# Kernel optimization log

Hardware: AMD Instinct MI355X
Metric: run time of the kernel (lower is better)

The kernel has to match this reference:

```python
import jax, jax.numpy as jnp
import numpy as np

B, C, F, T = 4, 64, 64, 128
IC = 32  # inter_channels = C // 2
EPS = 1e-5  # BatchNorm eps


def _conv1x1(x, w, b=None):
    # x: (B, Cin, H, W), w: (Cout, Cin)
    y = jnp.einsum('bchw,oc->bohw', x, w)
    if b is not None:
        y = y + b[None, :, None, None]
    return y


def _maxpool2(x):
    b, c, h, w = x.shape
    return x.reshape(b, c, h // 2, 2, w // 2, 2).max(axis=(3, 5))


def _pos_score(fsz, tsz, h2_w):
    # positional encoding is (fpos, tpos) in [0,1]; the 2->1 conv head makes the
    # pos_delta contribution separable: score(n,m) = s(n) - s(m)
    fpos = jnp.linspace(0.0, 1.0, fsz)
    tpos = jnp.linspace(0.0, 1.0, tsz)
    return (h2_w[0] * fpos[:, None] + h2_w[1] * tpos[None, :]).reshape(-1)


def setup_inputs() -> dict:
    key = jax.random.key(0)
    ks = jax.random.split(key, 16)
    s = 0.05
    inp = {
        'x': jax.random.normal(ks[0], (B, C, F, T), dtype=jnp.float32),
        'psi_w': jax.random.normal(ks[1], (IC, C)) * s,
        'psi_b': jax.random.normal(ks[2], (IC,)) * s,
        'theta_w': jax.random.normal(ks[3], (IC, C)) * s,
        'theta_b': jax.random.normal(ks[4], (IC,)) * s,
        'phi_w': jax.random.normal(ks[5], (IC, C)) * s,
        'phi_b': jax.random.normal(ks[6], (IC,)) * s,
        'h0_w': jax.random.normal(ks[7], (IC,)) * s,
        'h1_w': jax.random.normal(ks[8], (IC,)) * s,
        'h2_w': jax.random.normal(ks[9], (2,)) * s,
        'W_w': jax.random.normal(ks[10], (C, IC + 1)) * s,
        'W_b': jax.random.normal(ks[11], (C,)) * s,
        'bn_gamma': jax.random.normal(ks[12], (C,)) * s + 1.0,
        'bn_beta': jax.random.normal(ks[13], (C,)) * s,
        'bn_mean': jax.random.normal(ks[14], (C,)) * s,
        'bn_var': jax.random.uniform(ks[15], (C,), minval=0.5, maxval=1.5),
    }
    return inp


def reference(x, psi_w, psi_b, theta_w, theta_b, phi_w, phi_b,
              h0_w, h1_w, h2_w, W_w, W_b, bn_gamma, bn_beta, bn_mean, bn_var):
    Bs, Cs, Fs, Ts = x.shape
    N = Fs * Ts
    M = (Fs // 2) * (Ts // 2)

    psi_x = _maxpool2(_conv1x1(x, psi_w, psi_b))      # (B, IC, F/2, T/2)
    theta_x = _conv1x1(x, theta_w, theta_b)           # (B, IC, F, T)
    phi_x = _maxpool2(_conv1x1(x, phi_w, phi_b))      # (B, IC, F/2, T/2)

    # additive attention scores: relu(head0(theta) + head1(phi) + head2(pos_delta))
    t_score = jnp.einsum('bcft,c->bft', theta_x, h0_w).reshape(Bs, N)   # (B, N)
    p_score = jnp.einsum('bcft,c->bft', phi_x, h1_w).reshape(Bs, M)     # (B, M)
    a = _pos_score(Fs, Ts, h2_w)             # (N,) query pos contribution
    bpos = _pos_score(Fs // 2, Ts // 2, h2_w)  # (M,) key pos contribution
    f = jax.nn.relu((t_score + a[None, :])[:, :, None]
                    + (p_score - bpos[None, :])[:, None, :])  # (B, N, M)

    f_div = f / jnp.asarray(M, f.dtype)
    psi_flat = psi_x.reshape(Bs, IC, M)
    y = jnp.einsum('bnm,bcm->bcn', f_div, psi_flat).reshape(Bs, IC, Fs, Ts)

    # r_structure_type='zero' -> structure feature is zeros (1 extra channel)
    structure = jnp.zeros((Bs, 1, Fs, Ts), dtype=y.dtype)
    y = jnp.concatenate([y, structure], axis=1)       # (B, IC+1, F, T)

    wy = _conv1x1(y, W_w, W_b)                        # (B, C, F, T)
    inv = bn_gamma / jnp.sqrt(bn_var + EPS)
    wy = wy * inv[None, :, None, None] + (bn_beta - bn_mean * inv)[None, :, None, None]
    return wy + x
```

## Files before the change

### kernel.cpp

```cpp
#include <hip/hip_runtime.h>

#define B_ 4
#define C_ 64
#define F_ 64
#define T_ 128
#define IC_ 32
#define N_ 8192
#define M_ 2048

#define OFF_U      0
#define OFF_Z      32768
#define OFF_V      557056
#define OFF_VS     565248
#define OFF_Q01    573440
#define WS_FLOATS  1622528

__device__ __align__(16) float g_ws[WS_FLOATS];
__device__ int g_perm[B_ * M_];

__global__ __launch_bounds__(256) void k1(
    const float* __restrict__ x,
    const float* __restrict__ psi_w, const float* __restrict__ psi_b,
    const float* __restrict__ theta_w, const float* __restrict__ theta_b,
    const float* __restrict__ phi_w, const float* __restrict__ phi_b,
    const float* __restrict__ h0_w, const float* __restrict__ h1_w,
    const float* __restrict__ h2_w, const float* __restrict__ W_w)
{
    float* __restrict__ ws = g_ws;
    __shared__ __align__(16) float xs[4096];
    __shared__ __align__(16) float pw[2048];
    __shared__ __align__(16) float fw[2048];
    __shared__ __align__(16) float Wl[2048];
    __shared__ __align__(16) float pt[512];
    __shared__ float wt_l[64];

    const int tid = threadIdx.x;
    const int bid = blockIdx.x;
    const int b = bid >> 7;
    const int rem = bid & 127;
    const int fh = rem >> 2;
    const int q = rem & 3;
    const int c0 = q * 32;

    for (int idx = tid; idx < 1024; idx += 256) {
        const int c = idx >> 4, r2 = (idx >> 3) & 1, t4 = idx & 7;
        const float4 v = *(const float4*)&x[(((size_t)b * 64 + c) * 64 + (2 * fh + r2)) * 128 + c0 + 4 * t4];
        *(float4*)&xs[c * 64 + r2 * 32 + 4 * t4] = v;
    }
    for (int idx = tid; idx < 2048; idx += 256) {
        const int c4 = idx >> 7, o = (idx >> 2) & 31, j = idx & 3;
        pw[idx] = psi_w[o * 64 + 4 * c4 + j];
        fw[idx] = phi_w[o * 64 + 4 * c4 + j];
        const int c4w = idx >> 8, o64 = (idx >> 2) & 63, jw = idx & 3;
        Wl[idx] = W_w[o64 * 33 + 4 * c4w + jw];
    }
    if (tid < 64) {
        float acc = 0.f;
        for (int o2 = 0; o2 < 32; ++o2)
            acc += h0_w[o2] * theta_w[o2 * 64 + tid];
        wt_l[tid] = acc;
    }
    __syncthreads();

    const float h20 = h2_w[0], h21 = h2_w[1];

    {
        const int o = tid & 31, g = tid >> 5;
        const float pb = psi_b[o], fb = phi_b[o], h1 = h1_w[o];
        const float4* pw4 = (const float4*)pw;
        const float4* fw4 = (const float4*)fw;
        const float4* xs4 = (const float4*)xs;
        float sp[2][4] = {{0,0,0,0},{0,0,0,0}};
        float sf[2][4] = {{0,0,0,0},{0,0,0,0}};
        for (int c4 = 0; c4 < 16; ++c4) {
            const float4 pv = pw4[c4 * 32 + o];
            const float4 fv = fw4[c4 * 32 + o];
            const float* pvf = (const float*)&pv;
            const float* fvf = (const float*)&fv;
#pragma unroll
            for (int j = 0; j < 4; ++j) {
                const int c = 4 * c4 + j;
                const float4 r0 = xs4[c * 16 + g];
                const float4 r1 = xs4[c * 16 + 8 + g];
                const float wp = pvf[j], wf = fvf[j];
                sp[0][0] += wp * r0.x; sp[0][1] += wp * r0.y;
                sp[0][2] += wp * r1.x; sp[0][3] += wp * r1.y;
                sp[1][0] += wp * r0.z; sp[1][1] += wp * r0.w;
                sp[1][2] += wp * r1.z; sp[1][3] += wp * r1.w;
                sf[0][0] += wf * r0.x; sf[0][1] += wf * r0.y;
                sf[0][2] += wf * r1.x; sf[0][3] += wf * r1.y;
                sf[1][0] += wf * r0.z; sf[1][1] += wf * r0.w;
                sf[1][2] += wf * r1.z; sf[1][3] += wf * r1.w;
            }
        }
#pragma unroll
        for (int h = 0; h < 2; ++h) {
            const int hc = 2 * g + h;
            const float psiv = fmaxf(fmaxf(sp[h][0], sp[h][1]), fmaxf(sp[h][2], sp[h][3])) + pb;
            const float phiv = fmaxf(fmaxf(sf[h][0], sf[h][1]), fmaxf(sf[h][2], sf[h][3])) + fb;
            const int m = fh * 64 + q * 16 + hc;
            pt[hc * 32 + o] = psiv;
            float tv = h1 * phiv;
            for (int mask = 1; mask < 32; mask <<= 1)
                tv += __shfl_xor(tv, mask, 64);
            if (o == 0) {
                const float bpos = h20 * (fh * (1.0f / 31.0f))
                                 + h21 * ((q * 16 + hc) * (1.0f / 63.0f));
                ws[OFF_V + b * 2048 + m] = tv - bpos;
            }
        }
    }
    __syncthreads();

    {
        const int op = tid & 63, mseg = tid >> 6;
        const float4* Wl4 = (const float4*)Wl;
        const float4* pt4 = (const float4*)pt;
        float4 wreg[8];
#pragma unroll
        for (int c4 = 0; c4 < 8; ++c4)
            wreg[c4] = Wl4[c4 * 64 + op];
#pragma unroll
        for (int j = 0; j < 4; ++j) {
            const int ml = mseg * 4 + j;
            float acc = 0.f;
#pragma unroll
            for (int c4 = 0; c4 < 8; ++c4) {
                const float4 pv = pt4[ml * 8 + c4];
                acc += wreg[c4].x * pv.x + wreg[c4].y * pv.y
                     + wreg[c4].z * pv.z + wreg[c4].w * pv.w;
            }
            const int m = fh * 64 + q * 16 + ml;
            ws[OFF_Z + ((size_t)b * 2048 + m) * 64 + op] = acc;
        }
    }

    if (tid < 64) {
        const int r2 = tid >> 5, tl = tid & 31;
        float acc = 0.f;
        for (int c = 0; c < 64; ++c)
            acc += xs[c * 64 + r2 * 32 + tl] * wt_l[c];
        float tb_ = 0.f;
        for (int o2 = 0; o2 < 32; ++o2)
            tb_ += h0_w[o2] * theta_b[o2];
        const int f = 2 * fh + r2, tt = c0 + tl;
        const int n = f * 128 + tt;
        const float a = h20 * (f * (1.0f / 63.0f)) + h21 * (tt * (1.0f / 127.0f));
        ws[OFF_U + b * 8192 + n] = acc + tb_ + a;
    }
}

__global__ __launch_bounds__(256) void k2()
{
    float* __restrict__ ws = g_ws;
    __shared__ __align__(16) float vl[2048];
    __shared__ int part[256];
    const int tid = threadIdx.x;
    const int b = blockIdx.x >> 7, chunk = blockIdx.x & 127;
    const float* v = ws + OFF_V + b * 2048;
    for (int i = tid; i < 2048; i += 256) vl[i] = v[i];
    __syncthreads();

    const int ml = tid >> 4;
    const int jq = tid & 15;
    const int m = chunk * 16 + ml;
    const float vm = vl[m];
    int cnt = 0;
    const float4* v4 = (const float4*)vl;
#pragma unroll 4
    for (int i = 0; i < 32; ++i) {
        const int j4 = jq + 16 * i;
        const float4 vv = v4[j4];
        const int jb = j4 * 4;
        cnt += (vv.x > vm) || (vv.x == vm && (jb    ) < m);
        cnt += (vv.y > vm) || (vv.y == vm && (jb + 1) < m);
        cnt += (vv.z > vm) || (vv.z == vm && (jb + 2) < m);
        cnt += (vv.w > vm) || (vv.w == vm && (jb + 3) < m);
    }
    part[tid] = cnt;
    __syncthreads();
    if (tid < 16) {
        int r = 0;
#pragma unroll
        for (int j = 0; j < 16; ++j) r += part[tid * 16 + j];
        ws[OFF_VS + b * 2048 + r] = vl[chunk * 16 + tid];
        g_perm[b * 2048 + r] = chunk * 16 + tid;
    }
}

__global__ __launch_bounds__(512) void k3()
{
    float* __restrict__ ws = g_ws;
    __shared__ float wt0[8], wt1[8];
    const int tid = threadIdx.x;
    const int b = blockIdx.x >> 6, o = blockIdx.x & 63;

    const int* perm = g_perm + b * 2048;
    const float* vs = ws + OFF_VS + b * 2048;
    const float* zg = ws + OFF_Z + (size_t)b * 2048 * 64 + o;

    float zl[4], vlv[4];
    float s0 = 0.f, s1 = 0.f;
    const int base = tid * 4;
#pragma unroll
    for (int qq = 0; qq < 4; ++qq) {
        const int i = base + qq;
        const int mp = perm[i];
        const float z = zg[(size_t)mp * 64];
        const float vv = vs[i];
        zl[qq] = z; vlv[qq] = vv;
        s0 += z; s1 += vv * z;
    }

    float w0 = s0, w1 = s1;
    const int lane = tid & 63, wv = tid >> 6;
#pragma unroll
    for (int off = 1; off < 64; off <<= 1) {
        const float t0_ = __shfl_up(w0, off, 64);
        const float t1_ = __shfl_up(w1, off, 64);
        if (lane >= off) { w0 += t0_; w1 += t1_; }
    }
    if (lane == 63) { wt0[wv] = w0; wt1[wv] = w1; }
    __syncthreads();
    float base0 = 0.f, base1 = 0.f;
    for (int w = 0; w < wv; ++w) { base0 += wt0[w]; base1 += wt1[w]; }
    float r0 = w0 + base0 - s0, r1 = w1 + base1 - s1;

    float2* Q01 = (float2*)(ws + OFF_Q01) + (size_t)b * 2049 * 64;
#pragma unroll
    for (int qq = 0; qq < 4; ++qq) {
        r0 += zl[qq]; r1 += vlv[qq] * zl[qq];
        float2 p; p.x = r0; p.y = r1;
        Q01[(size_t)(base + qq + 1) * 64 + o] = p;
    }
    if (tid == 0) { float2 z2; z2.x = 0.f; z2.y = 0.f; Q01[o] = z2; }
}

__global__ __launch_bounds__(512) void k4(
    const float* __restrict__ x,
    const float* __restrict__ W_b,
    const float* __restrict__ bn_g, const float* __restrict__ bn_b,
    const float* __restrict__ bn_m, const float* __restrict__ bn_v,
    float* __restrict__ out)
{
    const float* __restrict__ ws = g_ws;
    __shared__ __align__(16) float vsl[2048];
    __shared__ float tileb[64 * 65];
    __shared__ int karr[64];
    __shared__ float uarr[64];

    const int tid = threadIdx.x;
    const int b = blockIdx.x >> 7, tile = blockIdx.x & 127;
    const int n0 = tile * 64;

    const float* vs = ws + OFF_VS + b * 2048;
    *(float4*)&vsl[tid * 4] = *(const float4*)&vs[tid * 4];
    __syncthreads();

    if (tid < 64) {
        const float u = ws[OFF_U + b * 8192 + n0 + tid];
        const float thr = -u;
        int lo = 0, hi = 2048;
        while (lo < hi) {
            const int mid = (lo + hi) >> 1;
            if (vsl[mid] > thr) lo = mid + 1; else hi = mid;
        }
        karr[tid] = lo;
        uarr[tid] = u;
    }
    __syncthreads();

    const int lane = tid & 63, w = tid >> 6;
    const float inv = bn_g[lane] * __frsqrt_rn(bn_v[lane] + 1e-5f);
    const float sft = W_b[lane] * inv + bn_b[lane] - bn_m[lane] * inv;
    const float2* Q01 = (const float2*)(ws + OFF_Q01) + (size_t)b * 2049 * 64;

    for (int nl = w; nl < 64; nl += 8) {
        const int k = karr[nl];
        const float u = uarr[nl];
        const float2 qv = Q01[(size_t)k * 64 + lane];
        const float raw = (u * qv.x + qv.y) * (1.0f / 2048.0f);
        tileb[lane * 65 + nl] = raw * inv + sft;
    }
    __syncthreads();

    for (int idx = tid; idx < 2048; idx += 512) {
        const int o = idx >> 5, j2 = idx & 31;
        const size_t gi = ((size_t)b * 64 + o) * 8192 + n0 + 2 * j2;
        const float2 xv = *(const float2*)&x[gi];
        float2 r;
        r.x = tileb[o * 65 + 2 * j2] + xv.x;
        r.y = tileb[o * 65 + 2 * j2 + 1] + xv.y;
        *(float2*)&out[gi] = r;
    }
}

extern "C" void kernel_launch(void* const* d_in, const int* in_sizes, int n_in,
                              void* d_out, int out_size, void* d_ws, size_t ws_size,
                              hipStream_t stream)
{
    (void)in_sizes; (void)n_in; (void)out_size; (void)d_ws; (void)ws_size;
    const float* x       = (const float*)d_in[0];
    const float* psi_w   = (const float*)d_in[1];
    const float* psi_b   = (const float*)d_in[2];
    const float* theta_w = (const float*)d_in[3];
    const float* theta_b = (const float*)d_in[4];
    const float* phi_w   = (const float*)d_in[5];
    const float* phi_b   = (const float*)d_in[6];
    const float* h0_w    = (const float*)d_in[7];
    const float* h1_w    = (const float*)d_in[8];
    const float* h2_w    = (const float*)d_in[9];
    const float* W_w     = (const float*)d_in[10];
    const float* W_b     = (const float*)d_in[11];
    const float* bn_g    = (const float*)d_in[12];
    const float* bn_b    = (const float*)d_in[13];
    const float* bn_m    = (const float*)d_in[14];
    const float* bn_v    = (const float*)d_in[15];
    float* out = (float*)d_out;

    k1<<<dim3(512), dim3(256), 0, stream>>>(x, psi_w, psi_b, theta_w, theta_b,
                                            phi_w, phi_b, h0_w, h1_w, h2_w, W_w);
    k2<<<dim3(512), dim3(256), 0, stream>>>();
    k3<<<dim3(256), dim3(512), 0, stream>>>();
    k4<<<dim3(512), dim3(512), 0, stream>>>(x, W_b, bn_g, bn_b, bn_m, bn_v, out);
}
```

Baseline: 120.2 us.

## Use bf16 MFMA for psi/phi and Z projections in k1 with swizzled LDS

Rewrites the first kernel to convert x and the weights to bf16 in swizzled shared memory and compute the psi/phi 1x1 convolutions and the W projection with 16x16x32 bf16 MFMA instructions instead of scalar FMA loops. Each block now covers 128 pixels, so the grid is halved. The Z workspace is transposed to channel-major so the gather in k3 reads contiguous rows per channel. This lowers arithmetic and LDS cost but brings bf16 rounding into the intermediate features, which can affect accuracy.

```diff
diff --git a/kernel.cpp b/kernel.cpp
--- a/kernel.cpp
+++ b/kernel.cpp
@@ -18,6 +18,23 @@
 __device__ __align__(16) float g_ws[WS_FLOATS];
 __device__ int g_perm[B_ * M_];
 
+typedef __attribute__((ext_vector_type(8))) short short8_t;
+typedef __attribute__((ext_vector_type(4))) float f32x4;
+
+__device__ __forceinline__ unsigned short f2bf(float f) {
+    unsigned b = __float_as_uint(f);
+    b += 0x7fffu + ((b >> 16) & 1u);
+    return (unsigned short)(b >> 16);
+}
+__device__ __forceinline__ float bf2f(unsigned short h) {
+    return __uint_as_float(((unsigned)h) << 16);
+}
+
+#define XSIDX(p, c)  ((((p) * 64) + (c)) ^ (((p) & 7) << 3))
+#define WAIDX(o, c)  ((((o) * 64) + (c)) ^ (((o) & 7) << 3))
+#define WZIDX(o, c)  ((((o) * 32) + (c)) ^ (((o) & 3) << 3))
+#define PSIDX(p, c)  ((((p) * 32) + (c)) ^ (((p) & 3) << 3))
+
 __global__ __launch_bounds__(256) void k1(
     const float* __restrict__ x,
     const float* __restrict__ psi_w, const float* __restrict__ psi_b,
@@ -27,126 +44,160 @@
     const float* __restrict__ h2_w, const float* __restrict__ W_w)
 {
     float* __restrict__ ws = g_ws;
-    __shared__ __align__(16) float xs[4096];
-    __shared__ __align__(16) float pw[2048];
-    __shared__ __align__(16) float fw[2048];
-    __shared__ __align__(16) float Wl[2048];
-    __shared__ __align__(16) float pt[512];
-    __shared__ float wt_l[64];
+    __shared__ __align__(16) unsigned short XS[128 * 64];
+    __shared__ __align__(16) unsigned short WA[64 * 64];
+    __shared__ __align__(16) unsigned short WZ[64 * 32];
+    __shared__ __align__(16) unsigned short PS[32 * 32];
+    __shared__ __align__(16) float pb[64];
+    __shared__ __align__(16) float h1l[32];
+    __shared__ __align__(16) float wtl[64];
+    __shared__ float vtmp[2][32];
 
     const int tid = threadIdx.x;
     const int bid = blockIdx.x;
-    const int b = bid >> 7;
-    const int rem = bid & 127;
-    const int fh = rem >> 2;
-    const int q = rem & 3;
-    const int c0 = q * 32;
-
-    for (int idx = tid; idx < 1024; idx += 256) {
-        const int c = idx >> 4, r2 = (idx >> 3) & 1, t4 = idx & 7;
-        const float4 v = *(const float4*)&x[(((size_t)b * 64 + c) * 64 + (2 * fh + r2)) * 128 + c0 + 4 * t4];
-        *(float4*)&xs[c * 64 + r2 * 32 + 4 * t4] = v;
-    }
-    for (int idx = tid; idx < 2048; idx += 256) {
-        const int c4 = idx >> 7, o = (idx >> 2) & 31, j = idx & 3;
-        pw[idx] = psi_w[o * 64 + 4 * c4 + j];
-        fw[idx] = phi_w[o * 64 + 4 * c4 + j];
-        const int c4w = idx >> 8, o64 = (idx >> 2) & 63, jw = idx & 3;
-        Wl[idx] = W_w[o64 * 33 + 4 * c4w + jw];
-    }
+    const int b = bid >> 6;
+    const int rem = bid & 63;
+    const int fh = rem >> 1;
+    const int hf = rem & 1;
+
+    const float h20 = h2_w[0], h21 = h2_w[1];
+
+    for (int it = 0; it < 2; ++it) {
+        const int u = it * 256 + tid;
+        const int colq = u & 15, r = (u >> 4) & 1, cq = u >> 5;
+        float4 xv[4];
+#pragma unroll
+        for (int j = 0; j < 4; ++j)
+            xv[j] = *(const float4*)&x[(((size_t)b * 64 + (4 * cq + j)) * 64 + (2 * fh + r)) * 128 + hf * 64 + 4 * colq];
+        const float* xf0 = (const float*)&xv[0];
+        const float* xf1 = (const float*)&xv[1];
+        const float* xf2 = (const float*)&xv[2];
+        const float* xf3 = (const float*)&xv[3];
+#pragma unroll
+        for (int i = 0; i < 4; ++i) {
+            const int p = r * 64 + 4 * colq + i;
+            short4 sv;
+            sv.x = (short)f2bf(xf0[i]); sv.y = (short)f2bf(xf1[i]);
+            sv.z = (short)f2bf(xf2[i]); sv.w = (short)f2bf(xf3[i]);
+            *(short4*)&XS[XSIDX(p, 4 * cq)] = sv;
+        }
+    }
+    for (int it = 0; it < 4; ++it) {
+        const int f4 = it * 256 + tid;
+        const int o2 = f4 >> 4;
+        const int cq = f4 & 15;
+        const float* src = (o2 < 32) ? &psi_w[o2 * 64 + 4 * cq]
+                                     : &phi_w[(o2 - 32) * 64 + 4 * cq];
+        const float4 wv = *(const float4*)src;
+        short4 sv;
+        sv.x = (short)f2bf(wv.x); sv.y = (short)f2bf(wv.y);
+        sv.z = (short)f2bf(wv.z); sv.w = (short)f2bf(wv.w);
+        *(short4*)&WA[WAIDX(o2, 4 * cq)] = sv;
+    }
+    for (int it = 0; it < 8; ++it) {
+        const int e = it * 256 + tid;
+        const int o64 = e >> 5, ic = e & 31;
+        WZ[WZIDX(o64, ic)] = f2bf(W_w[o64 * 33 + ic]);
+    }
+    if (tid < 64) pb[tid] = (tid < 32) ? psi_b[tid] : phi_b[tid - 32];
+    if (tid < 32) h1l[tid] = h1_w[tid];
     if (tid < 64) {
         float acc = 0.f;
         for (int o2 = 0; o2 < 32; ++o2)
             acc += h0_w[o2] * theta_w[o2 * 64 + tid];
-        wt_l[tid] = acc;
-    }
-    __syncthreads();
-
-    const float h20 = h2_w[0], h21 = h2_w[1];
+        wtl[tid] = acc;
+    }
+    __syncthreads();
+
+    const int w = tid >> 6, lane = tid & 63;
+    const int lo = lane & 15, hi = lane >> 4;
+
+    short8_t a0 = *(const short8_t*)&WA[WAIDX(16 * w + lo, hi * 8)];
+    short8_t a1 = *(const short8_t*)&WA[WAIDX(16 * w + lo, 32 + hi * 8)];
+    f32x4 acc[8];
+#pragma unroll
+    for (int t = 0; t < 8; ++t) { acc[t].x = 0.f; acc[t].y = 0.f; acc[t].z = 0.f; acc[t].w = 0.f; }
+#pragma unroll
+    for (int t = 0; t < 8; ++t) {
+        const short8_t b0 = *(const short8_t*)&XS[XSIDX(16 * t + lo, hi * 8)];
+        const short8_t b1 = *(const short8_t*)&XS[XSIDX(16 * t + lo, 32 + hi * 8)];
+        acc[t] = __builtin_amdgcn_mfma_f32_16x16x32_bf16(a0, b0, acc[t], 0, 0, 0);
+        acc[t] = __builtin_amdgcn_mfma_f32_16x16x32_bf16(a1, b1, acc[t], 0, 0, 0);
+    }
+
+    const int isPsi = (w < 2);
+    const int obase = (w & 1) * 16 + hi * 4;
+    const int pcj = lo >> 1;
+#pragma unroll
+    for (int t = 0; t < 4; ++t) {
+        const int pc = 8 * t + pcj;
+        float pv[4];
+#pragma unroll
+        for (int r = 0; r < 4; ++r) {
+            const float mx = fmaxf(acc[t][r], acc[t + 4][r]);
+            pv[r] = fmaxf(mx, __shfl_xor(mx, 1, 64)) + pb[(isPsi ? 0 : 32) + obase + r];
+        }
+        if (isPsi) {
+            if ((lane & 1) == 0) {
+                short4 sv;
+                sv.x = (short)f2bf(pv[0]); sv.y = (short)f2bf(pv[1]);
+                sv.z = (short)f2bf(pv[2]); sv.w = (short)f2bf(pv[3]);
+                *(short4*)&PS[PSIDX(pc, obase)] = sv;
+            }
+        } else {
+            float hp = h1l[obase] * pv[0] + h1l[obase + 1] * pv[1]
+                     + h1l[obase + 2] * pv[2] + h1l[obase + 3] * pv[3];
+            hp += __shfl_xor(hp, 16, 64);
+            hp += __shfl_xor(hp, 32, 64);
+            if (hi == 0 && (lane & 1) == 0)
+                vtmp[w - 2][pc] = hp;
+        }
+    }
+    __syncthreads();
+
+    if (tid < 32) {
+        const int pc = tid;
+        const int m = fh * 64 + hf * 32 + pc;
+        const float bpos = h20 * (fh * (1.0f / 31.0f))
+                         + h21 * ((hf * 32 + pc) * (1.0f / 63.0f));
+        ws[OFF_V + b * 2048 + m] = vtmp[0][pc] + vtmp[1][pc] - bpos;
+    }
 
     {
-        const int o = tid & 31, g = tid >> 5;
-        const float pb = psi_b[o], fb = phi_b[o], h1 = h1_w[o];
-        const float4* pw4 = (const float4*)pw;
-        const float4* fw4 = (const float4*)fw;
-        const float4* xs4 = (const float4*)xs;
-        float sp[2][4] = {{0,0,0,0},{0,0,0,0}};
-        float sf[2][4] = {{0,0,0,0},{0,0,0,0}};
-        for (int c4 = 0; c4 < 16; ++c4) {
-            const float4 pv = pw4[c4 * 32 + o];
-            const float4 fv = fw4[c4 * 32 + o];
-            const float* pvf = (const float*)&pv;
-            const float* fvf = (const float*)&fv;
-#pragma unroll
-            for (int j = 0; j < 4; ++j) {
-                const int c = 4 * c4 + j;
-                const float4 r0 = xs4[c * 16 + g];
-                const float4 r1 = xs4[c * 16 + 8 + g];
-                const float wp = pvf[j], wf = fvf[j];
-                sp[0][0] += wp * r0.x; sp[0][1] += wp * r0.y;
-                sp[0][2] += wp * r1.x; sp[0][3] += wp * r1.y;
-                sp[1][0] += wp * r0.z; sp[1][1] += wp * r0.w;
-                sp[1][2] += wp * r1.z; sp[1][3] += wp * r1.w;
-                sf[0][0] += wf * r0.x; sf[0][1] += wf * r0.y;
-                sf[0][2] += wf * r1.x; sf[0][3] += wf * r1.y;
-                sf[1][0] += wf * r0.z; sf[1][1] += wf * r0.w;
-                sf[1][2] += wf * r1.z; sf[1][3] += wf * r1.w;
-            }
-        }
-#pragma unroll
-        for (int h = 0; h < 2; ++h) {
-            const int hc = 2 * g + h;
-            const float psiv = fmaxf(fmaxf(sp[h][0], sp[h][1]), fmaxf(sp[h][2], sp[h][3])) + pb;
-            const float phiv = fmaxf(fmaxf(sf[h][0], sf[h][1]), fmaxf(sf[h][2], sf[h][3])) + fb;
-            const int m = fh * 64 + q * 16 + hc;
-            pt[hc * 32 + o] = psiv;
-            float tv = h1 * phiv;
-            for (int mask = 1; mask < 32; mask <<= 1)
-                tv += __shfl_xor(tv, mask, 64);
-            if (o == 0) {
-                const float bpos = h20 * (fh * (1.0f / 31.0f))
-                                 + h21 * ((q * 16 + hc) * (1.0f / 63.0f));
-                ws[OFF_V + b * 2048 + m] = tv - bpos;
-            }
-        }
-    }
-    __syncthreads();
+        const short8_t az = *(const short8_t*)&WZ[WZIDX(16 * w + lo, hi * 8)];
+#pragma unroll
+        for (int pt = 0; pt < 2; ++pt) {
+            const short8_t bz = *(const short8_t*)&PS[PSIDX(16 * pt + lo, hi * 8)];
+            f32x4 zc; zc.x = 0.f; zc.y = 0.f; zc.z = 0.f; zc.w = 0.f;
+            zc = __builtin_amdgcn_mfma_f32_16x16x32_bf16(az, bz, zc, 0, 0, 0);
+            const int m = fh * 64 + hf * 32 + 16 * pt + lo;
+#pragma unroll
+            for (int r = 0; r < 4; ++r)
+                ws[OFF_Z + ((size_t)b * 64 + 16 * w + hi * 4 + r) * 2048 + m] = zc[r];
+        }
+    }
 
     {
-        const int op = tid & 63, mseg = tid >> 6;
-        const float4* Wl4 = (const float4*)Wl;
-        const float4* pt4 = (const float4*)pt;
-        float4 wreg[8];
-#pragma unroll
-        for (int c4 = 0; c4 < 8; ++c4)
-            wreg[c4] = Wl4[c4 * 64 + op];
-#pragma unroll
-        for (int j = 0; j < 4; ++j) {
-            const int ml = mseg * 4 + j;
-            float acc = 0.f;
-#pragma unroll
-            for (int c4 = 0; c4 < 8; ++c4) {
-                const float4 pv = pt4[ml * 8 + c4];
-                acc += wreg[c4].x * pv.x + wreg[c4].y * pv.y
-                     + wreg[c4].z * pv.z + wreg[c4].w * pv.w;
-            }
-            const int m = fh * 64 + q * 16 + ml;
-            ws[OFF_Z + ((size_t)b * 2048 + m) * 64 + op] = acc;
-        }
-    }
-
-    if (tid < 64) {
-        const int r2 = tid >> 5, tl = tid & 31;
-        float acc = 0.f;
-        for (int c = 0; c < 64; ++c)
-            acc += xs[c * 64 + r2 * 32 + tl] * wt_l[c];
-        float tb_ = 0.f;
-        for (int o2 = 0; o2 < 32; ++o2)
-            tb_ += h0_w[o2] * theta_b[o2];
-        const int f = 2 * fh + r2, tt = c0 + tl;
-        const int n = f * 128 + tt;
-        const float a = h20 * (f * (1.0f / 63.0f)) + h21 * (tt * (1.0f / 127.0f));
-        ws[OFF_U + b * 8192 + n] = acc + tb_ + a;
+        const int ph = tid & 1, p = tid >> 1;
+        float ua = 0.f;
+#pragma unroll
+        for (int c4 = 0; c4 < 8; ++c4) {
+            const int c = ph * 32 + c4 * 4;
+            const short4 xv = *(const short4*)&XS[XSIDX(p, c)];
+            const float4 wv = *(const float4*)&wtl[c];
+            ua += wv.x * bf2f((unsigned short)xv.x) + wv.y * bf2f((unsigned short)xv.y)
+                + wv.z * bf2f((unsigned short)xv.z) + wv.w * bf2f((unsigned short)xv.w);
+        }
+        ua += __shfl_xor(ua, 1, 64);
+        if (ph == 0) {
+            float tb_ = 0.f;
+            for (int o2 = 0; o2 < 32; ++o2)
+                tb_ += h0_w[o2] * theta_b[o2];
+            const int f = 2 * fh + (p >> 6), tt = hf * 64 + (p & 63);
+            const int n = f * 128 + tt;
+            const float a = h20 * (f * (1.0f / 63.0f)) + h21 * (tt * (1.0f / 127.0f));
+            ws[OFF_U + b * 8192 + n] = ua + tb_ + a;
+        }
     }
 }
 
@@ -197,7 +248,7 @@
 
     const int* perm = g_perm + b * 2048;
     const float* vs = ws + OFF_VS + b * 2048;
-    const float* zg = ws + OFF_Z + (size_t)b * 2048 * 64 + o;
+    const float* zg = ws + OFF_Z + ((size_t)b * 64 + o) * 2048;
 
     float zl[4], vlv[4];
     float s0 = 0.f, s1 = 0.f;
@@ -206,7 +257,7 @@
     for (int qq = 0; qq < 4; ++qq) {
         const int i = base + qq;
         const int mp = perm[i];
-        const float z = zg[(size_t)mp * 64];
+        const float z = zg[mp];
         const float vv = vs[i];
         zl[qq] = z; vlv[qq] = vv;
         s0 += z; s1 += vv * z;
@@ -318,7 +369,7 @@
     const float* bn_v    = (const float*)d_in[15];
     float* out = (float*)d_out;
 
-    k1<<<dim3(512), dim3(256), 0, stream>>>(x, psi_w, psi_b, theta_w, theta_b,
+    k1<<<dim3(256), dim3(256), 0, stream>>>(x, psi_w, psi_b, theta_w, theta_b,
                                             phi_w, phi_b, h0_w, h1_w, h2_w, W_w);
     k2<<<dim3(512), dim3(256), 0, stream>>>();
     k3<<<dim3(256), dim3(512), 0, stream>>>();
```

Measured after the change: 113.5 us. 1.06x faster.
